# Kernel optimization log

Hardware: AMD Instinct MI355X
Metric: run time of the kernel (lower is better)

The kernel has to match this reference:

```python
import jax, jax.numpy as jnp
import numpy as np

EPS = 1e-5  # torch LayerNorm default
DT_RANK = 32  # ceil(d_model=512 / 16)


def layer_norm(x, g, b):
    mu = x.mean(-1, keepdims=True)
    var = x.var(-1, keepdims=True)
    return (x - mu) / jnp.sqrt(var + EPS) * g + b


def conv1d(x, w, b, pad):
    # x: (B, C, L), w: (O, I, K) -- torch Conv1d semantics
    y = jax.lax.conv_general_dilated(x, w, (1,), [(pad, pad)],
                                     dimension_numbers=('NCH', 'OIH', 'NCH'))
    return y + b[None, :, None]


def mamba(u, in_w, conv_w, conv_b, xproj_w, dt_w, dt_b, Alog, D, out_w, d_state, d_conv):
    # Faithful mamba_ssm Mamba block (no biases on in/x/out proj, RMS of official impl)
    Bsz, L, _ = u.shape
    xz = jnp.einsum('bld,ed->ble', u, in_w)          # (B, L, 2*Di)
    x, z = jnp.split(xz, 2, axis=-1)
    Di = x.shape[-1]
    # causal depthwise conv1d, truncated to L (padding=d_conv-1 on the left)
    xc = jax.lax.conv_general_dilated(x.transpose(0, 2, 1), conv_w[:, None, :], (1,),
                                      [(d_conv - 1, 0)],
                                      dimension_numbers=('NCH', 'OIH', 'NCH'),
                                      feature_group_count=Di)
    x = jax.nn.silu((xc + conv_b[None, :, None]).transpose(0, 2, 1))  # (B, L, Di)
    xdb = jnp.einsum('bld,ed->ble', x, xproj_w)       # (B, L, dt_rank + 2*N)
    dt = jax.nn.softplus(jnp.einsum('blr,dr->bld', xdb[..., :DT_RANK], dt_w) + dt_b)
    Bm = xdb[..., DT_RANK:DT_RANK + d_state]          # (B, L, N)
    Cm = xdb[..., DT_RANK + d_state:]                 # (B, L, N)
    A = -jnp.exp(Alog)                                # (Di, N)

    def step(h, ins):
        dt_t, x_t, B_t, C_t = ins                     # (B,Di),(B,Di),(B,N),(B,N)
        dA = jnp.exp(dt_t[..., None] * A)             # (B, Di, N)
        h = dA * h + (dt_t * x_t)[..., None] * B_t[:, None, :]
        y = (h * C_t[:, None, :]).sum(-1)             # (B, Di)
        return h, y

    h0 = jnp.zeros((Bsz, Di, d_state), u.dtype)
    xs = (dt.transpose(1, 0, 2), x.transpose(1, 0, 2),
          Bm.transpose(1, 0, 2), Cm.transpose(1, 0, 2))
    _, ys = jax.lax.scan(step, h0, xs)
    y = ys.transpose(1, 0, 2) + x * D                 # skip via D
    y = y * jax.nn.silu(z)
    return jnp.einsum('bld,od->blo', y, out_w)


def _forward(x, fe_w, fe_b, fe_ln_g, fe_ln_b, emb_ln_g, emb_ln_b,
             conv1_w, conv1_b, conv2_w, conv2_b,
             mf_in_w, mf_conv_w, mf_conv_b, mf_xproj_w, mf_dt_w, mf_dt_b, mf_Alog, mf_D, mf_out_w,
             mb_in_w, mb_conv_w, mb_conv_b, mb_xproj_w, mb_dt_w, mb_dt_b, mb_Alog, mb_D, mb_out_w,
             norm_g, norm_b, fc1_w, fc1_b, fc2_w, fc2_b):
    x = x.reshape(x.shape[0], 100, 23)
    # FrequencyEmbedding: rfft over a length-1 last dim == the signal itself; |.| then Linear+LN+ReLU
    id_mag = jnp.abs(x[..., :1])                      # (B, 100, 1)
    e = jax.nn.relu(layer_norm(id_mag @ fe_w.T + fe_b, fe_ln_g, fe_ln_b))
    id_embed = jax.nn.relu(layer_norm(e, emb_ln_g, emb_ln_b))  # outer LN+ReLU
    data = x[..., 1:].transpose(0, 2, 1)              # (B, 22, 100)
    f1 = jax.nn.relu(conv1d(data, conv1_w, conv1_b, 1))
    f2 = jax.nn.relu(conv1d(f1, conv2_w, conv2_b, 1)).transpose(0, 2, 1)  # (B,100,256)
    comb = jnp.concatenate([id_embed, f2], axis=-1)   # (B, 100, 512)
    fo = mamba(comb, mf_in_w, mf_conv_w, mf_conv_b, mf_xproj_w, mf_dt_w, mf_dt_b,
               mf_Alog, mf_D, mf_out_w, 16, 4)
    bo = mamba(comb[:, ::-1], mb_in_w, mb_conv_w, mb_conv_b, mb_xproj_w, mb_dt_w, mb_dt_b,
               mb_Alog, mb_D, mb_out_w, 8, 2)[:, ::-1]
    pooled = (fo + bo).max(axis=1)                    # (B, 512)
    pooled = layer_norm(pooled, norm_g, norm_b)       # self.norm (undefined in source; LN(512))
    h = jax.nn.relu(pooled @ fc1_w.T + fc1_b)
    return h @ fc2_w.T + fc2_b                        # (B, 4)


def setup_inputs() -> dict:
    key = jax.random.key(0)
    ks = iter(jax.random.split(key, 48))
    def n(shape, s=0.02):
        return jax.random.normal(next(ks), shape, jnp.float32) * s
    Di = 1024
    alog16 = jnp.log(jnp.tile(jnp.arange(1, 17, dtype=jnp.float32), (Di, 1)))
    alog8 = jnp.log(jnp.tile(jnp.arange(1, 9, dtype=jnp.float32), (Di, 1)))
    return {
        'x': jax.random.normal(next(ks), (512, 2300), jnp.float32),
        'fe_w': n((256, 1), 1.0), 'fe_b': jnp.zeros(256, jnp.float32),
        'fe_ln_g': jnp.ones(256, jnp.float32), 'fe_ln_b': jnp.zeros(256, jnp.float32),
        'emb_ln_g': jnp.ones(256, jnp.float32), 'emb_ln_b': jnp.zeros(256, jnp.float32),
        'conv1_w': n((128, 22, 3)), 'conv1_b': jnp.zeros(128, jnp.float32),
        'conv2_w': n((256, 128, 3)), 'conv2_b': jnp.zeros(256, jnp.float32),
        'mf_in_w': n((2 * Di, 512)), 'mf_conv_w': n((Di, 4)), 'mf_conv_b': jnp.zeros(Di, jnp.float32),
        'mf_xproj_w': n((32 + 2 * 16, Di)), 'mf_dt_w': n((Di, 32)), 'mf_dt_b': n((Di,), 0.1),
        'mf_Alog': alog16, 'mf_D': jnp.ones(Di, jnp.float32), 'mf_out_w': n((512, Di)),
        'mb_in_w': n((2 * Di, 512)), 'mb_conv_w': n((Di, 2)), 'mb_conv_b': jnp.zeros(Di, jnp.float32),
        'mb_xproj_w': n((32 + 2 * 8, Di)), 'mb_dt_w': n((Di, 32)), 'mb_dt_b': n((Di,), 0.1),
        'mb_Alog': alog8, 'mb_D': jnp.ones(Di, jnp.float32), 'mb_out_w': n((512, Di)),
        'norm_g': jnp.ones(512, jnp.float32), 'norm_b': jnp.zeros(512, jnp.float32),
        'fc1_w': n((128, 512)), 'fc1_b': jnp.zeros(128, jnp.float32),
        'fc2_w': n((4, 128)), 'fc2_b': jnp.zeros(4, jnp.float32),
    }


def reference(x, fe_w, fe_b, fe_ln_g, fe_ln_b, emb_ln_g, emb_ln_b,
              conv1_w, conv1_b, conv2_w, conv2_b,
              mf_in_w, mf_conv_w, mf_conv_b, mf_xproj_w, mf_dt_w, mf_dt_b, mf_Alog, mf_D, mf_out_w,
              mb_in_w, mb_conv_w, mb_conv_b, mb_xproj_w, mb_dt_w, mb_dt_b, mb_Alog, mb_D, mb_out_w,
              norm_g, norm_b, fc1_w, fc1_b, fc2_w, fc2_b):
    return _forward(x, fe_w, fe_b, fe_ln_g, fe_ln_b, emb_ln_g, emb_ln_b,
                    conv1_w, conv1_b, conv2_w, conv2_b,
                    mf_in_w, mf_conv_w, mf_conv_b, mf_xproj_w, mf_dt_w, mf_dt_b, mf_Alog, mf_D, mf_out_w,
                    mb_in_w, mb_conv_w, mb_conv_b, mb_xproj_w, mb_dt_w, mb_dt_b, mb_Alog, mb_D, mb_out_w,
                    norm_g, norm_b, fc1_w, fc1_b, fc2_w, fc2_b)
```

## Files before the change

### kernel.cpp

```cpp
#include <hip/hip_runtime.h>
#include <cstddef>
#include <cstdint>

#define BSZ 512
#define SEQ 100

typedef __bf16 bf16_t;
typedef __attribute__((ext_vector_type(8))) __bf16 bf16x8;
typedef __attribute__((ext_vector_type(4))) float f32x4;

__device__ __forceinline__ float sigmoidf_(float v){ return 1.f/(1.f + __expf(-v)); }
__device__ __forceinline__ float siluf_(float v){ return v * sigmoidf_(v); }
__device__ __forceinline__ float softplusf_(float v){ return (v > 20.f) ? v : __logf(1.f + __expf(v)); }

__global__ __launch_bounds__(256) void cvt_bf16_kernel(
    const float* __restrict__ src, bf16_t* __restrict__ dst, int n)
{
    int i = blockIdx.x*256 + threadIdx.x;
    if (i < n) dst[i] = (bf16_t)src[i];
}

__global__ __launch_bounds__(256) void prep_outw_kernel(
    const float* __restrict__ of, const float* __restrict__ ob, bf16_t* __restrict__ W)
{
    int i = blockIdx.x*256 + threadIdx.x;
    if (i < 512*2048){
        int o = i >> 11, k = i & 2047;
        W[i] = (bf16_t)((k < 1024) ? of[o*1024 + k] : ob[o*1024 + (k - 1024)]);
    }
}

__global__ __launch_bounds__(256) void prep_convw_kernel(
    const float* __restrict__ c1w, const float* __restrict__ c2w,
    bf16_t* __restrict__ W1p, bf16_t* __restrict__ W2p)
{
    int i = blockIdx.x*256 + threadIdx.x;
    if (i < 128*96){
        int o = i / 96, kk = i - o*96, k = kk >> 5, c = kk & 31;
        W1p[i] = (c < 22) ? (bf16_t)c1w[(o*22 + c)*3 + k] : (bf16_t)0.f;
    }
    if (i < 256*384){
        int o = i / 384, kk = i - o*384, k = kk >> 7, c = kk & 127;
        W2p[i] = (bf16_t)c2w[(o*128 + c)*3 + k];
    }
}

__global__ __launch_bounds__(256) void fe0_kernel(
    const float* __restrict__ x,
    const float* __restrict__ fe_w, const float* __restrict__ fe_b,
    const float* __restrict__ g1, const float* __restrict__ b1,
    const float* __restrict__ g2, const float* __restrict__ b2,
    bf16_t* __restrict__ comb, bf16_t* __restrict__ F0pad, bf16_t* __restrict__ F1pad)
{
    const int b = blockIdx.x;
    const int t = threadIdx.x;
    const int wv = t >> 6, lane = t & 63;

    float few[4], feb[4], lg1[4], lb1[4], lg2[4], lb2[4];
    #pragma unroll
    for (int q = 0; q < 4; ++q){
        int j = lane + 64*q;
        few[q] = fe_w[j]; feb[q] = fe_b[j];
        lg1[q] = g1[j];  lb1[q] = b1[j];
        lg2[q] = g2[j];  lb2[q] = b2[j];
    }
    for (int l = wv; l < SEQ; l += 4){
        float m = fabsf(x[(size_t)(b*SEQ + l)*23]);
        float e[4];
        float s1 = 0.f, s2 = 0.f;
        #pragma unroll
        for (int q = 0; q < 4; ++q){ e[q] = m*few[q] + feb[q]; s1 += e[q]; s2 += e[q]*e[q]; }
        #pragma unroll
        for (int off = 32; off > 0; off >>= 1){ s1 += __shfl_xor(s1, off); s2 += __shfl_xor(s2, off); }
        float mean = s1 * (1.f/256.f);
        float rstd = rsqrtf(s2*(1.f/256.f) - mean*mean + 1e-5f);
        s1 = 0.f; s2 = 0.f;
        #pragma unroll
        for (int q = 0; q < 4; ++q){
            e[q] = fmaxf((e[q]-mean)*rstd*lg1[q] + lb1[q], 0.f);
            s1 += e[q]; s2 += e[q]*e[q];
        }
        #pragma unroll
        for (int off = 32; off > 0; off >>= 1){ s1 += __shfl_xor(s1, off); s2 += __shfl_xor(s2, off); }
        mean = s1 * (1.f/256.f);
        rstd = rsqrtf(s2*(1.f/256.f) - mean*mean + 1e-5f);
        #pragma unroll
        for (int q = 0; q < 4; ++q){
            float v = fmaxf((e[q]-mean)*rstd*lg2[q] + lb2[q], 0.f);
            comb[(size_t)(b*SEQ + l)*512 + lane + 64*q] = (bf16_t)v;
        }
    }

    for (int idx = t; idx < 102*32; idx += 256){
        int r = idx >> 5, c = idx & 31;
        float v = 0.f;
        if (r >= 1 && r <= SEQ && c < 22) v = x[(size_t)(b*SEQ + r - 1)*23 + 1 + c];
        F0pad[(size_t)(b*102 + r)*32 + c] = (bf16_t)v;
    }
    if (t < 128) F1pad[(size_t)(b*102 + 0)*128 + t] = (bf16_t)0.f;
    else F1pad[(size_t)(b*102 + 101)*128 + (t - 128)] = (bf16_t)0.f;
}

__global__ __launch_bounds__(256) void gemm_conv_kernel(
    const bf16_t* __restrict__ Abase, int lda, int Az,
    const bf16_t* __restrict__ W, int K, int N,
    const float* __restrict__ bias,
    bf16_t* __restrict__ Cbase, int ldc, int Cb, int coff, int noff, int Mtot)
{
    __shared__ bf16_t As[128*32];
    __shared__ bf16_t Ws[128*32];
    const bf16_t* A = Abase + (size_t)blockIdx.z * Az;
    const int t = threadIdx.x;
    const int lane = t & 63, w = t >> 6;
    const int n0 = blockIdx.y * 128;
    const int rsub = lane >> 2, csub = lane & 3;
    const int col = lane & 15, quad = lane >> 4;
    const int wOffM = (w & 1) * 64, wOffN = (w >> 1) * 64;

    f32x4 acc[4][4];
    #pragma unroll
    for (int i = 0; i < 4; ++i)
        #pragma unroll
        for (int j = 0; j < 4; ++j)
            acc[i][j] = (f32x4){0.f, 0.f, 0.f, 0.f};

    for (int k0 = 0; k0 < K; k0 += 32){
        __syncthreads();
        #pragma unroll
        for (int q = 0; q < 2; ++q){
            const int rt = w*32 + q*16 + rsub;
            const int lq = csub ^ ((rt >> 1) & 3);
            int ra = (rt < Mtot) ? rt : (Mtot - 1);
            const bf16_t* ga = A + (size_t)ra*lda + k0 + lq*8;
            __builtin_amdgcn_global_load_lds(
                (const __attribute__((address_space(1))) void*)ga,
                (__attribute__((address_space(3))) void*)&As[(w*32 + q*16)*32], 16, 0, 0);
            const bf16_t* gw = W + (size_t)(n0 + rt)*K + k0 + lq*8;
            __builtin_amdgcn_global_load_lds(
                (const __attribute__((address_space(1))) void*)gw,
                (__attribute__((address_space(3))) void*)&Ws[(w*32 + q*16)*32], 16, 0, 0);
        }
        __syncthreads();

        bf16x8 af[4], bfv[4];
        #pragma unroll
        for (int i = 0; i < 4; ++i){
            const int ra = wOffM + i*16 + col;
            af[i]  = *(const bf16x8*)&As[ra*32 + (quad ^ ((ra >> 1) & 3))*8];
            const int rb = wOffN + i*16 + col;
            bfv[i] = *(const bf16x8*)&Ws[rb*32 + (quad ^ ((rb >> 1) & 3))*8];
        }
        #pragma unroll
        for (int i = 0; i < 4; ++i)
            #pragma unroll
            for (int j = 0; j < 4; ++j)
                acc[i][j] = __builtin_amdgcn_mfma_f32_16x16x32_bf16(af[i], bfv[j], acc[i][j], 0, 0, 0);
    }

    #pragma unroll
    for (int i = 0; i < 4; ++i){
        const int gmb = wOffM + i*16 + quad*4;
        #pragma unroll
        for (int j = 0; j < 4; ++j){
            const int gn = n0 + wOffN + j*16 + col;
            const float bb = bias[gn];
            #pragma unroll
            for (int r = 0; r < 4; ++r){
                const int gm = gmb + r;
                if (gm < Mtot){
                    float v = fmaxf(acc[i][j][r] + bb, 0.f);
                    Cbase[((size_t)blockIdx.z*Cb + coff + gm)*ldc + noff + gn] = (bf16_t)v;
                }
            }
        }
    }
}

__global__ __launch_bounds__(256) void gemm_in_kernel(
    const bf16_t* __restrict__ A, int lda, int Mtot,
    const bf16_t* __restrict__ W, int K,
    bf16_t* __restrict__ xy, bf16_t* __restrict__ z)
{
    __shared__ bf16_t As[128*32];
    __shared__ bf16_t Ws[128*32];
    const int t = threadIdx.x;
    const int lane = t & 63, w = t >> 6;
    const int m0 = blockIdx.x * 128, n0 = blockIdx.y * 128;
    const int rsub = lane >> 2, csub = lane & 3;
    const int col = lane & 15, quad = lane >> 4;
    const int wOffM = (w & 1) * 64, wOffN = (w >> 1) * 64;

    f32x4 acc[4][4];
    #pragma unroll
    for (int i = 0; i < 4; ++i)
        #pragma unroll
        for (int j = 0; j < 4; ++j)
            acc[i][j] = (f32x4){0.f, 0.f, 0.f, 0.f};

    for (int k0 = 0; k0 < K; k0 += 32){
        __syncthreads();
        #pragma unroll
        for (int q = 0; q < 2; ++q){
            const int rt = w*32 + q*16 + rsub;
            const int lq = csub ^ ((rt >> 1) & 3);
            int ra = m0 + rt; ra = (ra < Mtot) ? ra : (Mtot - 1);
            const bf16_t* ga = A + (size_t)ra*lda + k0 + lq*8;
            __builtin_amdgcn_global_load_lds(
                (const __attribute__((address_space(1))) void*)ga,
                (__attribute__((address_space(3))) void*)&As[(w*32 + q*16)*32], 16, 0, 0);
            const bf16_t* gw = W + (size_t)(n0 + rt)*K + k0 + lq*8;
            __builtin_amdgcn_global_load_lds(
                (const __attribute__((address_space(1))) void*)gw,
                (__attribute__((address_space(3))) void*)&Ws[(w*32 + q*16)*32], 16, 0, 0);
        }
        __syncthreads();

        bf16x8 af[4], bfv[4];
        #pragma unroll
        for (int i = 0; i < 4; ++i){
            const int ra = wOffM + i*16 + col;
            af[i]  = *(const bf16x8*)&As[ra*32 + (quad ^ ((ra >> 1) & 3))*8];
            const int rb = wOffN + i*16 + col;
            bfv[i] = *(const bf16x8*)&Ws[rb*32 + (quad ^ ((rb >> 1) & 3))*8];
        }
        #pragma unroll
        for (int i = 0; i < 4; ++i)
            #pragma unroll
            for (int j = 0; j < 4; ++j)
                acc[i][j] = __builtin_amdgcn_mfma_f32_16x16x32_bf16(af[i], bfv[j], acc[i][j], 0, 0, 0);
    }

    #pragma unroll
    for (int i = 0; i < 4; ++i){
        const int gmb = m0 + wOffM + i*16 + quad*4;
        #pragma unroll
        for (int j = 0; j < 4; ++j){
            const int gn = n0 + wOffN + j*16 + col;
            const int half = gn >> 11, within = gn & 2047;
            const size_t colx = (size_t)(half*1024 + (within & 1023));
            bf16_t* dst = (within < 1024) ? xy : z;
            #pragma unroll
            for (int r = 0; r < 4; ++r){
                const int gm = gmb + r;
                if (gm < Mtot)
                    dst[(size_t)gm*2048 + colx] = (bf16_t)acc[i][j][r];
            }
        }
    }
}

__global__ __launch_bounds__(256) void gemm_out_kernel(
    const bf16_t* __restrict__ A, int Mtot,
    const bf16_t* __restrict__ W,
    float* __restrict__ C)
{
    __shared__ bf16_t As[128*32];
    __shared__ bf16_t Ws[128*32];
    const int t = threadIdx.x;
    const int lane = t & 63, w = t >> 6;
    const int m0 = blockIdx.x * 128, n0 = blockIdx.y * 128;
    const int rsub = lane >> 2, csub = lane & 3;
    const int col = lane & 15, quad = lane >> 4;
    const int wOffM = (w & 1) * 64, wOffN = (w >> 1) * 64;
    const int K = 2048;

    f32x4 acc[4][4];
    #pragma unroll
    for (int i = 0; i < 4; ++i)
        #pragma unroll
        for (int j = 0; j < 4; ++j)
            acc[i][j] = (f32x4){0.f, 0.f, 0.f, 0.f};

    for (int k0 = 0; k0 < K; k0 += 32){
        __syncthreads();
        #pragma unroll
        for (int q = 0; q < 2; ++q){
            const int rt = w*32 + q*16 + rsub;
            const int lq = csub ^ ((rt >> 1) & 3);
            int ra = m0 + rt; ra = (ra < Mtot) ? ra : (Mtot - 1);
            const bf16_t* ga = A + (size_t)ra*K + k0 + lq*8;
            __builtin_amdgcn_global_load_lds(
                (const __attribute__((address_space(1))) void*)ga,
                (__attribute__((address_space(3))) void*)&As[(w*32 + q*16)*32], 16, 0, 0);
            const bf16_t* gw = W + (size_t)(n0 + rt)*K + k0 + lq*8;
            __builtin_amdgcn_global_load_lds(
                (const __attribute__((address_space(1))) void*)gw,
                (__attribute__((address_space(3))) void*)&Ws[(w*32 + q*16)*32], 16, 0, 0);
        }
        __syncthreads();

        bf16x8 af[4], bfv[4];
        #pragma unroll
        for (int i = 0; i < 4; ++i){
            const int ra = wOffM + i*16 + col;
            af[i]  = *(const bf16x8*)&As[ra*32 + (quad ^ ((ra >> 1) & 3))*8];
            const int rb = wOffN + i*16 + col;
            bfv[i] = *(const bf16x8*)&Ws[rb*32 + (quad ^ ((rb >> 1) & 3))*8];
        }
        #pragma unroll
        for (int i = 0; i < 4; ++i)
            #pragma unroll
            for (int j = 0; j < 4; ++j)
                acc[i][j] = __builtin_amdgcn_mfma_f32_16x16x32_bf16(af[i], bfv[j], acc[i][j], 0, 0, 0);
    }

    #pragma unroll
    for (int i = 0; i < 4; ++i){
        const int gmb = m0 + wOffM + i*16 + quad*4;
        #pragma unroll
        for (int j = 0; j < 4; ++j){
            const int gn = n0 + wOffN + j*16 + col;
            #pragma unroll
            for (int r = 0; r < 4; ++r){
                const int gm = gmb + r;
                if (gm < Mtot)
                    C[(size_t)gm*512 + gn] = acc[i][j][r];
            }
        }
    }
}

__global__ __launch_bounds__(256) void gemm_x_kernel(
    const bf16_t* __restrict__ xy,
    const bf16_t* __restrict__ Wf, const bf16_t* __restrict__ Wb,
    float* __restrict__ C)
{
    __shared__ bf16_t As[128*32];
    __shared__ bf16_t Ws[64*32];
    const int half = blockIdx.y;
    const bf16_t* A = xy + half*1024;
    const bf16_t* W = half ? Wb : Wf;
    const int N = half ? 48 : 64;
    const int t = threadIdx.x;
    const int lane = t & 63, w = t >> 6;
    const int m0 = blockIdx.x * 128;
    const int rsub = lane >> 2, csub = lane & 3;
    const int col = lane & 15, quad = lane >> 4;

    f32x4 acc[2][4];
    #pragma unroll
    for (int i = 0; i < 2; ++i)
        #pragma unroll
        for (int j = 0; j < 4; ++j)
            acc[i][j] = (f32x4){0.f, 0.f, 0.f, 0.f};

    for (int k0 = 0; k0 < 1024; k0 += 32){
        __syncthreads();
        #pragma unroll
        for (int q = 0; q < 2; ++q){
            const int rt = q*64 + w*16 + rsub;
            const int lq = csub ^ ((rt >> 1) & 3);
            const bf16_t* ga = A + (size_t)(m0 + rt)*2048 + k0 + lq*8;
            __builtin_amdgcn_global_load_lds(
                (const __attribute__((address_space(1))) void*)ga,
                (__attribute__((address_space(3))) void*)&As[(q*64 + w*16)*32], 16, 0, 0);
        }
        {
            const int rt = w*16 + rsub;
            const int lq = csub ^ ((rt >> 1) & 3);
            int rw = (rt < N) ? rt : (N - 1);
            const bf16_t* gw = W + (size_t)rw*1024 + k0 + lq*8;
            __builtin_amdgcn_global_load_lds(
                (const __attribute__((address_space(1))) void*)gw,
                (__attribute__((address_space(3))) void*)&Ws[(w*16)*32], 16, 0, 0);
        }
        __syncthreads();

        bf16x8 af[2], bfv[4];
        #pragma unroll
        for (int i = 0; i < 2; ++i){
            const int ra = w*32 + i*16 + col;
            af[i]  = *(const bf16x8*)&As[ra*32 + (quad ^ ((ra >> 1) & 3))*8];
        }
        #pragma unroll
        for (int j = 0; j < 4; ++j){
            const int rb = j*16 + col;
            bfv[j] = *(const bf16x8*)&Ws[rb*32 + (quad ^ ((rb >> 1) & 3))*8];
        }
        #pragma unroll
        for (int i = 0; i < 2; ++i)
            #pragma unroll
            for (int j = 0; j < 4; ++j)
                acc[i][j] = __builtin_amdgcn_mfma_f32_16x16x32_bf16(af[i], bfv[j], acc[i][j], 0, 0, 0);
    }

    #pragma unroll
    for (int i = 0; i < 2; ++i){
        const int gmb = m0 + w*32 + i*16 + quad*4;
        #pragma unroll
        for (int j = 0; j < 4; ++j){
            const int gn = j*16 + col;
            if (gn < N){
                #pragma unroll
                for (int r = 0; r < 4; ++r)
                    C[(size_t)(gmb + r)*128 + half*64 + gn] = acc[i][j][r];
            }
        }
    }
}

__global__ __launch_bounds__(256) void dt_kernel(
    const float* __restrict__ xdb,
    const float* __restrict__ dtwf, const float* __restrict__ dtbf,
    const float* __restrict__ dtwb, const float* __restrict__ dtbb,
    bf16_t* __restrict__ dtb)
{
    const int half = blockIdx.y >> 3;
    const int d = (blockIdx.y & 7)*128 + (threadIdx.x & 127);
    const int mslot = threadIdx.x >> 7;
    const int m0 = blockIdx.x * 16;
    __shared__ float sd[16*32];
    for (int i = threadIdx.x; i < 16*32; i += 256){
        int r = i >> 5, c = i & 31;
        sd[i] = xdb[(size_t)(m0 + r)*128 + half*64 + c];
    }
    const float* dw = half ? dtwb : dtwf;
    float w[32];
    #pragma unroll
    for (int r = 0; r < 32; ++r) w[r] = dw[d*32 + r];
    const float db = half ? dtbb[d] : dtbf[d];
    __syncthreads();
    #pragma unroll
    for (int i = 0; i < 8; ++i){
        const int row = mslot + i*2;
        const float* rp = &sd[row*32];
        float a = db;
        #pragma unroll
        for (int r = 0; r < 32; ++r) a += w[r]*rp[r];
        dtb[(size_t)(m0 + row)*2048 + half*1024 + d] = (bf16_t)softplusf_(a);
    }
}

template<int DC, bool REV>
__device__ __forceinline__ void conv_dev(bf16_t* base, const float* wsrc, float bias)
{
    float w[DC];
    #pragma unroll
    for (int k = 0; k < DC; ++k) w[k] = wsrc[k];
    float hist[DC-1];
    #pragma unroll
    for (int k = 0; k < DC-1; ++k) hist[k] = 0.f;
    const int step = REV ? -1 : 1;
    int l = REV ? (SEQ-1) : 0;
    for (int t0 = 0; t0 < SEQ; t0 += 10){
        float v[10];
        #pragma unroll
        for (int i = 0; i < 10; ++i) v[i] = (float)base[(size_t)(l + step*i)*2048];
        float o[10];
        #pragma unroll
        for (int i = 0; i < 10; ++i){
            float a = bias + w[DC-1]*v[i];
            #pragma unroll
            for (int j = 1; j < DC; ++j) a += w[DC-1-j]*hist[j-1];
            #pragma unroll
            for (int j = DC-2; j >= 1; --j) hist[j] = hist[j-1];
            hist[0] = v[i];
            o[i] = siluf_(a);
        }
        #pragma unroll
        for (int i = 0; i < 10; ++i)
            base[(size_t)(l + step*i)*2048] = (bf16_t)o[i];
        l += step*10;
    }
}

__global__ __launch_bounds__(256) void conv_silu_kernel(
    bf16_t* __restrict__ xy,
    const float* __restrict__ cwf, const float* __restrict__ cbf,
    const float* __restrict__ cwb, const float* __restrict__ cbb)
{
    const int gid = blockIdx.x*256 + threadIdx.x;
    const int b = gid >> 11, d2 = gid & 2047;
    const int half = d2 >> 10, d = d2 & 1023;
    bf16_t* base = xy + (size_t)b*SEQ*2048 + d2;
    if (half == 0) conv_dev<4, false>(base, cwf + d*4, cbf[d]);
    else           conv_dev<2, true >(base, cwb + d*2, cbb[d]);
}

template<int DS, bool REV>
__device__ __forceinline__ void scan_dev(
    bf16_t* __restrict__ xybase, const bf16_t* __restrict__ zbase,
    const bf16_t* __restrict__ tbase, const float* __restrict__ sx,
    const float* __restrict__ Arow, float Dd)
{
    float Av[DS], h[DS];
    #pragma unroll
    for (int s = 0; s < DS; ++s){ Av[s] = -__expf(Arow[s]); h[s] = 0.f; }
    bool structured = true;
    #pragma unroll
    for (int s = 1; s < DS; ++s)
        structured = structured && (fabsf(Av[s] - (float)(s+1)*Av[0]) <= 1e-4f*(float)(s+1));
    const float A0 = Av[0];
    const int step = REV ? -1 : 1;

    if (structured){
        int l = REV ? (SEQ-1) : 0;
        for (int t0 = 0; t0 < SEQ; t0 += 10){
            float xr[10], zr[10], tr[10];
            #pragma unroll
            for (int i = 0; i < 10; ++i){
                const size_t li = (size_t)(l + step*i);
                xr[i] = (float)xybase[li*2048];
                zr[i] = (float)zbase[li*2048];
                tr[i] = (float)tbase[li*2048];
            }
            #pragma unroll
            for (int i = 0; i < 10; ++i){
                const int li = l + step*i;
                const float4* sxl4 = (const float4*)&sx[li*2*DS];
                const float dtv = tr[i];
                const float dtx = dtv * xr[i];
                const float r = __expf(dtv*A0);
                float rp = r;
                float yv = 0.f;
                #pragma unroll
                for (int s4 = 0; s4 < DS/4; ++s4){
                    float4 Bv = sxl4[s4];
                    float4 Cv = sxl4[DS/4 + s4];
                    h[s4*4+0] = rp*h[s4*4+0] + dtx*Bv.x; yv += h[s4*4+0]*Cv.x; rp *= r;
                    h[s4*4+1] = rp*h[s4*4+1] + dtx*Bv.y; yv += h[s4*4+1]*Cv.y; rp *= r;
                    h[s4*4+2] = rp*h[s4*4+2] + dtx*Bv.z; yv += h[s4*4+2]*Cv.z; rp *= r;
                    h[s4*4+3] = rp*h[s4*4+3] + dtx*Bv.w; yv += h[s4*4+3]*Cv.w; rp *= r;
                }
                yv += xr[i]*Dd;
                yv *= siluf_(zr[i]);
                xybase[(size_t)li*2048] = (bf16_t)yv;
            }
            l += step*10;
        }
    } else {
        int l = REV ? (SEQ-1) : 0;
        for (int t0 = 0; t0 < SEQ; t0 += 10){
            float xr[10], zr[10], tr[10];
            #pragma unroll
            for (int i = 0; i < 10; ++i){
                const size_t li = (size_t)(l + step*i);
                xr[i] = (float)xybase[li*2048];
                zr[i] = (float)zbase[li*2048];
                tr[i] = (float)tbase[li*2048];
            }
            #pragma unroll
            for (int i = 0; i < 10; ++i){
                const int li = l + step*i;
                const float4* sxl4 = (const float4*)&sx[li*2*DS];
                const float dtv = tr[i];
                const float dtx = dtv * xr[i];
                float yv = 0.f;
                #pragma unroll
                for (int s4 = 0; s4 < DS/4; ++s4){
                    float4 Bv = sxl4[s4];
                    float4 Cv = sxl4[DS/4 + s4];
                    h[s4*4+0] = __expf(dtv*Av[s4*4+0])*h[s4*4+0] + dtx*Bv.x; yv += h[s4*4+0]*Cv.x;
                    h[s4*4+1] = __expf(dtv*Av[s4*4+1])*h[s4*4+1] + dtx*Bv.y; yv += h[s4*4+1]*Cv.y;
                    h[s4*4+2] = __expf(dtv*Av[s4*4+2])*h[s4*4+2] + dtx*Bv.z; yv += h[s4*4+2]*Cv.z;
                    h[s4*4+3] = __expf(dtv*Av[s4*4+3])*h[s4*4+3] + dtx*Bv.w; yv += h[s4*4+3]*Cv.w;
                }
                yv += xr[i]*Dd;
                yv *= siluf_(zr[i]);
                xybase[(size_t)li*2048] = (bf16_t)yv;
            }
            l += step*10;
        }
    }
}

__global__ __launch_bounds__(256) void scan_kernel(
    bf16_t* __restrict__ xy, const bf16_t* __restrict__ z,
    const bf16_t* __restrict__ dtb, const float* __restrict__ xdb,
    const float* __restrict__ Alogf, const float* __restrict__ Dpf,
    const float* __restrict__ Alogb, const float* __restrict__ Dpb)
{
    const int b = blockIdx.x >> 3, s8 = blockIdx.x & 7;
    __shared__ float sx[SEQ*32];
    const float4* src = (const float4*)(xdb + (size_t)b*SEQ*128);
    float4* dst = (float4*)sx;

    if (s8 < 4){
        for (int i = threadIdx.x; i < SEQ*8; i += 256){
            int row = i >> 3, c = i & 7;
            dst[row*8 + c] = src[row*32 + 8 + c];
        }
        const int d = (s8 << 8) + threadIdx.x;
        __syncthreads();
        scan_dev<16, false>(
            xy  + (size_t)b*SEQ*2048 + d,
            z   + (size_t)b*SEQ*2048 + d,
            dtb + (size_t)b*SEQ*2048 + d,
            sx, Alogf + d*16, Dpf[d]);
    } else {
        for (int i = threadIdx.x; i < SEQ*4; i += 256){
            int row = i >> 2, c = i & 3;
            dst[row*4 + c] = src[row*32 + 24 + c];
        }
        const int d = ((s8 - 4) << 8) + threadIdx.x;
        __syncthreads();
        scan_dev<8, true>(
            xy  + (size_t)b*SEQ*2048 + 1024 + d,
            z   + (size_t)b*SEQ*2048 + 1024 + d,
            dtb + (size_t)b*SEQ*2048 + 1024 + d,
            sx, Alogb + d*8, Dpb[d]);
    }
}

__global__ __launch_bounds__(256) void head_kernel(
    const float* __restrict__ acc,
    const float* __restrict__ ng, const float* __restrict__ nb,
    const float* __restrict__ w1, const float* __restrict__ b1,
    const float* __restrict__ w2, const float* __restrict__ b2,
    float* __restrict__ out)
{
    const int b = blockIdx.x, t = threadIdx.x;
    __shared__ float4 sm4[256];
    __shared__ float sp[512];
    __shared__ float sh2[256];
    __shared__ float sh[128];
    __shared__ float red1[4], red2[4];
    const float* base = acc + (size_t)b*SEQ*512;

    {
        const int c4 = t & 127, lh = t >> 7;
        float4 m = make_float4(-3.4e38f, -3.4e38f, -3.4e38f, -3.4e38f);
        for (int l = lh*50; l < lh*50 + 50; ++l){
            float4 v = ((const float4*)(base + (size_t)l*512))[c4];
            m.x = fmaxf(m.x, v.x); m.y = fmaxf(m.y, v.y);
            m.z = fmaxf(m.z, v.z); m.w = fmaxf(m.w, v.w);
        }
        sm4[t] = m;
    }
    __syncthreads();
    if (t < 128){
        float4 a = sm4[t], c = sm4[t + 128];
        ((float4*)sp)[t] = make_float4(fmaxf(a.x,c.x), fmaxf(a.y,c.y),
                                       fmaxf(a.z,c.z), fmaxf(a.w,c.w));
    }
    __syncthreads();

    float s1 = 0.f, s2 = 0.f;
    for (int o = t; o < 512; o += 256){ float v = sp[o]; s1 += v; s2 += v*v; }
    #pragma unroll
    for (int off = 32; off > 0; off >>= 1){ s1 += __shfl_xor(s1, off); s2 += __shfl_xor(s2, off); }
    const int wv = t >> 6, lane = t & 63;
    if (lane == 0){ red1[wv] = s1; red2[wv] = s2; }
    __syncthreads();
    if (t == 0){
        float a = 0.f, c = 0.f;
        for (int i = 0; i < 4; ++i){ a += red1[i]; c += red2[i]; }
        float mean = a * (1.f/512.f);
        float var = c * (1.f/512.f) - mean*mean;
        red1[0] = mean; red2[0] = rsqrtf(var + 1e-5f);
    }
    __syncthreads();
    const float mean = red1[0], rstd = red2[0];
    for (int o = t; o < 512; o += 256) sp[o] = (sp[o]-mean)*rstd*ng[o] + nb[o];
    __syncthreads();

    {
        const int o = t & 127, half = t >> 7;
        const float4* wrow = (const float4*)(w1 + (size_t)o*512 + half*256);
        const float4* sp4 = (const float4*)sp + half*64;
        float s = 0.f;
        #pragma unroll 8
        for (int j = 0; j < 64; ++j){
            float4 a = sp4[j], wq = wrow[j];
            s += a.x*wq.x + a.y*wq.y + a.z*wq.z + a.w*wq.w;
        }
        sh2[t] = s;
    }
    __syncthreads();
    if (t < 128) sh[t] = fmaxf(sh2[t] + sh2[t + 128] + b1[t], 0.f);
    __syncthreads();
    if (t < 4){
        float a = b2[t];
        for (int j = 0; j < 128; ++j) a += sh[j]*w2[t*128 + j];
        out[b*4 + t] = a;
    }
}

extern "C" void kernel_launch(void* const* d_in, const int* in_sizes, int n_in,
                              void* d_out, int out_size, void* d_ws, size_t ws_size,
                              hipStream_t stream)
{
    (void)in_sizes; (void)n_in; (void)out_size;
    const float* x        = (const float*)d_in[0];
    const float* fe_w     = (const float*)d_in[1];
    const float* fe_b     = (const float*)d_in[2];
    const float* fe_ln_g  = (const float*)d_in[3];
    const float* fe_ln_b  = (const float*)d_in[4];
    const float* emb_ln_g = (const float*)d_in[5];
    const float* emb_ln_b = (const float*)d_in[6];
    const float* conv1_w  = (const float*)d_in[7];
    const float* conv1_b  = (const float*)d_in[8];
    const float* conv2_w  = (const float*)d_in[9];
    const float* conv2_b  = (const float*)d_in[10];
    const float* mf_in_w  = (const float*)d_in[11];
    const float* mf_conv_w= (const float*)d_in[12];
    const float* mf_conv_b= (const float*)d_in[13];
    const float* mf_xproj = (const float*)d_in[14];
    const float* mf_dt_w  = (const float*)d_in[15];
    const float* mf_dt_b  = (const float*)d_in[16];
    const float* mf_Alog  = (const float*)d_in[17];
    const float* mf_D     = (const float*)d_in[18];
    const float* mf_out_w = (const float*)d_in[19];
    const float* mb_in_w  = (const float*)d_in[20];
    const float* mb_conv_w= (const float*)d_in[21];
    const float* mb_conv_b= (const float*)d_in[22];
    const float* mb_xproj = (const float*)d_in[23];
    const float* mb_dt_w  = (const float*)d_in[24];
    const float* mb_dt_b  = (const float*)d_in[25];
    const float* mb_Alog  = (const float*)d_in[26];
    const float* mb_D     = (const float*)d_in[27];
    const float* mb_out_w = (const float*)d_in[28];
    const float* norm_g   = (const float*)d_in[29];
    const float* norm_b   = (const float*)d_in[30];
    const float* fc1_w    = (const float*)d_in[31];
    const float* fc1_b    = (const float*)d_in[32];
    const float* fc2_w    = (const float*)d_in[33];
    const float* fc2_b    = (const float*)d_in[34];
    float* out = (float*)d_out;

    char* p = (char*)d_ws;
    bf16_t* w_in   = (bf16_t*)p; p += (size_t)4096*512*sizeof(bf16_t);
    bf16_t* w_out  = (bf16_t*)p; p += (size_t)512*2048*sizeof(bf16_t);
    bf16_t* w_xpf  = (bf16_t*)p; p += (size_t)64*1024*sizeof(bf16_t);
    bf16_t* w_xpb  = (bf16_t*)p; p += (size_t)48*1024*sizeof(bf16_t);
    bf16_t* W1p    = (bf16_t*)p; p += (size_t)128*96*sizeof(bf16_t);
    bf16_t* W2p    = (bf16_t*)p; p += (size_t)256*384*sizeof(bf16_t);
    bf16_t* comb_all = (bf16_t*)p; p += (size_t)BSZ*SEQ*512*sizeof(bf16_t);
    const size_t fixed_bytes = (size_t)(p - (char*)d_ws);

    const size_t per_b = (size_t)SEQ * (2048*2 + 2048*2 + 2048*2 + 128*4);
    const size_t budget = (ws_size > fixed_bytes) ? (ws_size - fixed_bytes) : 0;
    int Bc = BSZ;
    while (Bc > 64 && (size_t)Bc * per_b > budget) Bc >>= 1;
    const int nch = BSZ / Bc;
    const int M = Bc * SEQ;

    bf16_t* F0pad = (bf16_t*)p;
    bf16_t* F1pad = F0pad + (size_t)BSZ*102*32;
    bf16_t* xy   = (bf16_t*)p;               p += (size_t)M*2048*sizeof(bf16_t);
    bf16_t* z    = (bf16_t*)p;               p += (size_t)M*2048*sizeof(bf16_t);
    bf16_t* dtb  = (bf16_t*)p;               p += (size_t)M*2048*sizeof(bf16_t);
    float*  xdb  = (float*)p;
    float*  accb = (float*)dtb;

    cvt_bf16_kernel<<<(2048*512+255)/256, 256, 0, stream>>>(mf_in_w, w_in, 2048*512);
    cvt_bf16_kernel<<<(2048*512+255)/256, 256, 0, stream>>>(mb_in_w, w_in + (size_t)2048*512, 2048*512);
    prep_outw_kernel<<<(512*2048+255)/256, 256, 0, stream>>>(mf_out_w, mb_out_w, w_out);
    cvt_bf16_kernel<<<(64*1024+255)/256,  256, 0, stream>>>(mf_xproj, w_xpf, 64*1024);
    cvt_bf16_kernel<<<(48*1024+255)/256,  256, 0, stream>>>(mb_xproj, w_xpb, 48*1024);
    prep_convw_kernel<<<(256*384+255)/256, 256, 0, stream>>>(conv1_w, conv2_w, W1p, W2p);

    fe0_kernel<<<BSZ, 256, 0, stream>>>(x, fe_w, fe_b, fe_ln_g, fe_ln_b,
        emb_ln_g, emb_ln_b, comb_all, F0pad, F1pad);
    gemm_conv_kernel<<<dim3(1, 1, BSZ), 256, 0, stream>>>(
        F0pad, 32, 102*32, W1p, 96, 128, conv1_b, F1pad, 128, 102, 1, 0, SEQ);
    gemm_conv_kernel<<<dim3(1, 2, BSZ), 256, 0, stream>>>(
        F1pad, 128, 102*128, W2p, 384, 256, conv2_b, comb_all, 512, 100, 0, 256, SEQ);

    const int gm128 = M / 128;

    for (int c = 0; c < nch; ++c){
        const size_t b0 = (size_t)c * Bc;
        const bf16_t* comb = comb_all + b0*SEQ*512;

        gemm_in_kernel<<<dim3(gm128, 32), 256, 0, stream>>>(comb, 512, M, w_in, 512, xy, z);
        conv_silu_kernel<<<Bc*2048/256, 256, 0, stream>>>(xy, mf_conv_w, mf_conv_b,
                                                          mb_conv_w, mb_conv_b);
        gemm_x_kernel<<<dim3(gm128, 2), 256, 0, stream>>>(xy, w_xpf, w_xpb, xdb);
        dt_kernel<<<dim3(M/16, 16), 256, 0, stream>>>(xdb, mf_dt_w, mf_dt_b,
                                                      mb_dt_w, mb_dt_b, dtb);
        scan_kernel<<<Bc*8, 256, 0, stream>>>(xy, z, dtb, xdb,
                                              mf_Alog, mf_D, mb_Alog, mb_D);
        gemm_out_kernel<<<dim3(gm128, 4), 256, 0, stream>>>(xy, M, w_out, accb);
        head_kernel<<<Bc, 256, 0, stream>>>(accb, norm_g, norm_b, fc1_w, fc1_b,
                                            fc2_w, fc2_b, out + b0*4);
    }
}
```

Baseline: 1.598 ms.

## Double K-step per barrier in GEMMs and balance fwd/bwd scan work per block

The in- and out-projection GEMMs now load two 32-wide K slices into separate LDS buffers per iteration, which halves the number of barrier pairs at the cost of twice the LDS per block. The scan kernel now gives every block 128 forward (16-state) channels and 128 backward (8-state) channels instead of putting only one direction in each block, which evens out per-block latency. The scan body is also refactored into a single templated core with the structured and unstructured A paths chosen at compile time, which may reduce code duplication and register pressure.

```diff
diff --git a/kernel.cpp b/kernel.cpp
--- a/kernel.cpp
+++ b/kernel.cpp
@@ -181,8 +181,8 @@
     const bf16_t* __restrict__ W, int K,
     bf16_t* __restrict__ xy, bf16_t* __restrict__ z)
 {
-    __shared__ bf16_t As[128*32];
-    __shared__ bf16_t Ws[128*32];
+    __shared__ bf16_t As[2][128*32];
+    __shared__ bf16_t Ws[2][128*32];
     const int t = threadIdx.x;
     const int lane = t & 63, w = t >> 6;
     const int m0 = blockIdx.x * 128, n0 = blockIdx.y * 128;
@@ -197,37 +197,43 @@
         for (int j = 0; j < 4; ++j)
             acc[i][j] = (f32x4){0.f, 0.f, 0.f, 0.f};
 
-    for (int k0 = 0; k0 < K; k0 += 32){
+    for (int k0 = 0; k0 < K; k0 += 64){
         __syncthreads();
         #pragma unroll
-        for (int q = 0; q < 2; ++q){
-            const int rt = w*32 + q*16 + rsub;
-            const int lq = csub ^ ((rt >> 1) & 3);
-            int ra = m0 + rt; ra = (ra < Mtot) ? ra : (Mtot - 1);
-            const bf16_t* ga = A + (size_t)ra*lda + k0 + lq*8;
-            __builtin_amdgcn_global_load_lds(
-                (const __attribute__((address_space(1))) void*)ga,
-                (__attribute__((address_space(3))) void*)&As[(w*32 + q*16)*32], 16, 0, 0);
-            const bf16_t* gw = W + (size_t)(n0 + rt)*K + k0 + lq*8;
-            __builtin_amdgcn_global_load_lds(
-                (const __attribute__((address_space(1))) void*)gw,
-                (__attribute__((address_space(3))) void*)&Ws[(w*32 + q*16)*32], 16, 0, 0);
+        for (int hh = 0; hh < 2; ++hh){
+            #pragma unroll
+            for (int q = 0; q < 2; ++q){
+                const int rt = w*32 + q*16 + rsub;
+                const int lq = csub ^ ((rt >> 1) & 3);
+                int ra = m0 + rt; ra = (ra < Mtot) ? ra : (Mtot - 1);
+                const bf16_t* ga = A + (size_t)ra*lda + k0 + hh*32 + lq*8;
+                __builtin_amdgcn_global_load_lds(
+                    (const __attribute__((address_space(1))) void*)ga,
+                    (__attribute__((address_space(3))) void*)&As[hh][(w*32 + q*16)*32], 16, 0, 0);
+                const bf16_t* gw = W + (size_t)(n0 + rt)*K + k0 + hh*32 + lq*8;
+                __builtin_amdgcn_global_load_lds(
+                    (const __attribute__((address_space(1))) void*)gw,
+                    (__attribute__((address_space(3))) void*)&Ws[hh][(w*32 + q*16)*32], 16, 0, 0);
+            }
         }
         __syncthreads();
 
-        bf16x8 af[4], bfv[4];
-        #pragma unroll
-        for (int i = 0; i < 4; ++i){
-            const int ra = wOffM + i*16 + col;
-            af[i]  = *(const bf16x8*)&As[ra*32 + (quad ^ ((ra >> 1) & 3))*8];
-            const int rb = wOffN + i*16 + col;
-            bfv[i] = *(const bf16x8*)&Ws[rb*32 + (quad ^ ((rb >> 1) & 3))*8];
-        }
-        #pragma unroll
-        for (int i = 0; i < 4; ++i)
-            #pragma unroll
-            for (int j = 0; j < 4; ++j)
-                acc[i][j] = __builtin_amdgcn_mfma_f32_16x16x32_bf16(af[i], bfv[j], acc[i][j], 0, 0, 0);
+        #pragma unroll
+        for (int hh = 0; hh < 2; ++hh){
+            bf16x8 af[4], bfv[4];
+            #pragma unroll
+            for (int i = 0; i < 4; ++i){
+                const int ra = wOffM + i*16 + col;
+                af[i]  = *(const bf16x8*)&As[hh][ra*32 + (quad ^ ((ra >> 1) & 3))*8];
+                const int rb = wOffN + i*16 + col;
+                bfv[i] = *(const bf16x8*)&Ws[hh][rb*32 + (quad ^ ((rb >> 1) & 3))*8];
+            }
+            #pragma unroll
+            for (int i = 0; i < 4; ++i)
+                #pragma unroll
+                for (int j = 0; j < 4; ++j)
+                    acc[i][j] = __builtin_amdgcn_mfma_f32_16x16x32_bf16(af[i], bfv[j], acc[i][j], 0, 0, 0);
+        }
     }
 
     #pragma unroll
@@ -254,8 +260,8 @@
     const bf16_t* __restrict__ W,
     float* __restrict__ C)
 {
-    __shared__ bf16_t As[128*32];
-    __shared__ bf16_t Ws[128*32];
+    __shared__ bf16_t As[2][128*32];
+    __shared__ bf16_t Ws[2][128*32];
     const int t = threadIdx.x;
     const int lane = t & 63, w = t >> 6;
     const int m0 = blockIdx.x * 128, n0 = blockIdx.y * 128;
@@ -271,37 +277,43 @@
         for (int j = 0; j < 4; ++j)
             acc[i][j] = (f32x4){0.f, 0.f, 0.f, 0.f};
 
-    for (int k0 = 0; k0 < K; k0 += 32){
+    for (int k0 = 0; k0 < K; k0 += 64){
         __syncthreads();
         #pragma unroll
-        for (int q = 0; q < 2; ++q){
-            const int rt = w*32 + q*16 + rsub;
-            const int lq = csub ^ ((rt >> 1) & 3);
-            int ra = m0 + rt; ra = (ra < Mtot) ? ra : (Mtot - 1);
-            const bf16_t* ga = A + (size_t)ra*K + k0 + lq*8;
-            __builtin_amdgcn_global_load_lds(
-                (const __attribute__((address_space(1))) void*)ga,
-                (__attribute__((address_space(3))) void*)&As[(w*32 + q*16)*32], 16, 0, 0);
-            const bf16_t* gw = W + (size_t)(n0 + rt)*K + k0 + lq*8;
-            __builtin_amdgcn_global_load_lds(
-                (const __attribute__((address_space(1))) void*)gw,
-                (__attribute__((address_space(3))) void*)&Ws[(w*32 + q*16)*32], 16, 0, 0);
+        for (int hh = 0; hh < 2; ++hh){
+            #pragma unroll
+            for (int q = 0; q < 2; ++q){
+                const int rt = w*32 + q*16 + rsub;
+                const int lq = csub ^ ((rt >> 1) & 3);
+                int ra = m0 + rt; ra = (ra < Mtot) ? ra : (Mtot - 1);
+                const bf16_t* ga = A + (size_t)ra*K + k0 + hh*32 + lq*8;
+                __builtin_amdgcn_global_load_lds(
+                    (const __attribute__((address_space(1))) void*)ga,
+                    (__attribute__((address_space(3))) void*)&As[hh][(w*32 + q*16)*32], 16, 0, 0);
+                const bf16_t* gw = W + (size_t)(n0 + rt)*K + k0 + hh*32 + lq*8;
+                __builtin_amdgcn_global_load_lds(
+                    (const __attribute__((address_space(1))) void*)gw,
+                    (__attribute__((address_space(3))) void*)&Ws[hh][(w*32 + q*16)*32], 16, 0, 0);
+            }
         }
         __syncthreads();
 
-        bf16x8 af[4], bfv[4];
-        #pragma unroll
-        for (int i = 0; i < 4; ++i){
-            const int ra = wOffM + i*16 + col;
-            af[i]  = *(const bf16x8*)&As[ra*32 + (quad ^ ((ra >> 1) & 3))*8];
-            const int rb = wOffN + i*16 + col;
-            bfv[i] = *(const bf16x8*)&Ws[rb*32 + (quad ^ ((rb >> 1) & 3))*8];
-        }
-        #pragma unroll
-        for (int i = 0; i < 4; ++i)
-            #pragma unroll
-            for (int j = 0; j < 4; ++j)
-                acc[i][j] = __builtin_amdgcn_mfma_f32_16x16x32_bf16(af[i], bfv[j], acc[i][j], 0, 0, 0);
+        #pragma unroll
+        for (int hh = 0; hh < 2; ++hh){
+            bf16x8 af[4], bfv[4];
+            #pragma unroll
+            for (int i = 0; i < 4; ++i){
+                const int ra = wOffM + i*16 + col;
+                af[i]  = *(const bf16x8*)&As[hh][ra*32 + (quad ^ ((ra >> 1) & 3))*8];
+                const int rb = wOffN + i*16 + col;
+                bfv[i] = *(const bf16x8*)&Ws[hh][rb*32 + (quad ^ ((rb >> 1) & 3))*8];
+            }
+            #pragma unroll
+            for (int i = 0; i < 4; ++i)
+                #pragma unroll
+                for (int j = 0; j < 4; ++j)
+                    acc[i][j] = __builtin_amdgcn_mfma_f32_16x16x32_bf16(af[i], bfv[j], acc[i][j], 0, 0, 0);
+        }
     }
 
     #pragma unroll
@@ -477,42 +489,38 @@
     else           conv_dev<2, true >(base, cwb + d*2, cbb[d]);
 }
 
-template<int DS, bool REV>
-__device__ __forceinline__ void scan_dev(
+template<int DS, bool REV, bool STRUCT>
+__device__ __forceinline__ void scan_core(
     bf16_t* __restrict__ xybase, const bf16_t* __restrict__ zbase,
     const bf16_t* __restrict__ tbase, const float* __restrict__ sx,
-    const float* __restrict__ Arow, float Dd)
-{
-    float Av[DS], h[DS];
-    #pragma unroll
-    for (int s = 0; s < DS; ++s){ Av[s] = -__expf(Arow[s]); h[s] = 0.f; }
-    bool structured = true;
-    #pragma unroll
-    for (int s = 1; s < DS; ++s)
-        structured = structured && (fabsf(Av[s] - (float)(s+1)*Av[0]) <= 1e-4f*(float)(s+1));
+    const float* __restrict__ Av, float Dd)
+{
+    float h[DS];
+    #pragma unroll
+    for (int s = 0; s < DS; ++s) h[s] = 0.f;
+    const int step = REV ? -1 : 1;
     const float A0 = Av[0];
-    const int step = REV ? -1 : 1;
-
-    if (structured){
-        int l = REV ? (SEQ-1) : 0;
-        for (int t0 = 0; t0 < SEQ; t0 += 10){
-            float xr[10], zr[10], tr[10];
-            #pragma unroll
-            for (int i = 0; i < 10; ++i){
-                const size_t li = (size_t)(l + step*i);
-                xr[i] = (float)xybase[li*2048];
-                zr[i] = (float)zbase[li*2048];
-                tr[i] = (float)tbase[li*2048];
-            }
-            #pragma unroll
-            for (int i = 0; i < 10; ++i){
-                const int li = l + step*i;
-                const float4* sxl4 = (const float4*)&sx[li*2*DS];
-                const float dtv = tr[i];
-                const float dtx = dtv * xr[i];
+    int l = REV ? (SEQ-1) : 0;
+
+    for (int t0 = 0; t0 < SEQ; t0 += 10){
+        float xr[10], zr[10], tr[10];
+        #pragma unroll
+        for (int i = 0; i < 10; ++i){
+            const size_t li = (size_t)(l + step*i);
+            xr[i] = (float)xybase[li*2048];
+            zr[i] = (float)zbase[li*2048];
+            tr[i] = (float)tbase[li*2048];
+        }
+        #pragma unroll
+        for (int i = 0; i < 10; ++i){
+            const int li = l + step*i;
+            const float4* sxl4 = (const float4*)&sx[li*2*DS];
+            const float dtv = tr[i];
+            const float dtx = dtv * xr[i];
+            float yv = 0.f;
+            if (STRUCT){
                 const float r = __expf(dtv*A0);
                 float rp = r;
-                float yv = 0.f;
                 #pragma unroll
                 for (int s4 = 0; s4 < DS/4; ++s4){
                     float4 Bv = sxl4[s4];
@@ -522,30 +530,7 @@
                     h[s4*4+2] = rp*h[s4*4+2] + dtx*Bv.z; yv += h[s4*4+2]*Cv.z; rp *= r;
                     h[s4*4+3] = rp*h[s4*4+3] + dtx*Bv.w; yv += h[s4*4+3]*Cv.w; rp *= r;
                 }
-                yv += xr[i]*Dd;
-                yv *= siluf_(zr[i]);
-                xybase[(size_t)li*2048] = (bf16_t)yv;
-            }
-            l += step*10;
-        }
-    } else {
-        int l = REV ? (SEQ-1) : 0;
-        for (int t0 = 0; t0 < SEQ; t0 += 10){
-            float xr[10], zr[10], tr[10];
-            #pragma unroll
-            for (int i = 0; i < 10; ++i){
-                const size_t li = (size_t)(l + step*i);
-                xr[i] = (float)xybase[li*2048];
-                zr[i] = (float)zbase[li*2048];
-                tr[i] = (float)tbase[li*2048];
-            }
-            #pragma unroll
-            for (int i = 0; i < 10; ++i){
-                const int li = l + step*i;
-                const float4* sxl4 = (const float4*)&sx[li*2*DS];
-                const float dtv = tr[i];
-                const float dtx = dtv * xr[i];
-                float yv = 0.f;
+            } else {
                 #pragma unroll
                 for (int s4 = 0; s4 < DS/4; ++s4){
                     float4 Bv = sxl4[s4];
@@ -555,13 +540,30 @@
                     h[s4*4+2] = __expf(dtv*Av[s4*4+2])*h[s4*4+2] + dtx*Bv.z; yv += h[s4*4+2]*Cv.z;
                     h[s4*4+3] = __expf(dtv*Av[s4*4+3])*h[s4*4+3] + dtx*Bv.w; yv += h[s4*4+3]*Cv.w;
                 }
-                yv += xr[i]*Dd;
-                yv *= siluf_(zr[i]);
-                xybase[(size_t)li*2048] = (bf16_t)yv;
-            }
-            l += step*10;
-        }
-    }
+            }
+            yv += xr[i]*Dd;
+            yv *= siluf_(zr[i]);
+            xybase[(size_t)li*2048] = (bf16_t)yv;
+        }
+        l += step*10;
+    }
+}
+
+template<int DS, bool REV>
+__device__ __forceinline__ void scan_dev(
+    bf16_t* __restrict__ xybase, const bf16_t* __restrict__ zbase,
+    const bf16_t* __restrict__ tbase, const float* __restrict__ sx,
+    const float* __restrict__ Arow, float Dd)
+{
+    float Av[DS];
+    #pragma unroll
+    for (int s = 0; s < DS; ++s) Av[s] = -__expf(Arow[s]);
+    bool structured = true;
+    #pragma unroll
+    for (int s = 1; s < DS; ++s)
+        structured = structured && (fabsf(Av[s] - (float)(s+1)*Av[0]) <= 1e-4f*(float)(s+1));
+    if (structured) scan_core<DS, REV, true >(xybase, zbase, tbase, sx, Av, Dd);
+    else            scan_core<DS, REV, false>(xybase, zbase, tbase, sx, Av, Dd);
 }
 
 __global__ __launch_bounds__(256) void scan_kernel(
@@ -571,34 +573,33 @@
     const float* __restrict__ Alogb, const float* __restrict__ Dpb)
 {
     const int b = blockIdx.x >> 3, s8 = blockIdx.x & 7;
-    __shared__ float sx[SEQ*32];
+    const int t = threadIdx.x;
+    __shared__ float sxF[SEQ*32];
+    __shared__ float sxB[SEQ*16];
     const float4* src = (const float4*)(xdb + (size_t)b*SEQ*128);
-    float4* dst = (float4*)sx;
-
-    if (s8 < 4){
-        for (int i = threadIdx.x; i < SEQ*8; i += 256){
+
+    {
+        float4* dstF = (float4*)sxF;
+        for (int i = t; i < SEQ*8; i += 256){
             int row = i >> 3, c = i & 7;
-            dst[row*8 + c] = src[row*32 + 8 + c];
-        }
-        const int d = (s8 << 8) + threadIdx.x;
-        __syncthreads();
-        scan_dev<16, false>(
-            xy  + (size_t)b*SEQ*2048 + d,
-            z   + (size_t)b*SEQ*2048 + d,
-            dtb + (size_t)b*SEQ*2048 + d,
-            sx, Alogf + d*16, Dpf[d]);
+            dstF[row*8 + c] = src[row*32 + 8 + c];
+        }
+        float4* dstB = (float4*)sxB;
+        for (int i = t; i < SEQ*4; i += 256){
+            int row = i >> 2, c = i & 3;
+            dstB[row*4 + c] = src[row*32 + 24 + c];
+        }
+    }
+    __syncthreads();
+
+    if (t < 128){
+        const int d = s8*128 + t;
+        const size_t off = (size_t)b*SEQ*2048 + d;
+        scan_dev<16, false>(xy + off, z + off, dtb + off, sxF, Alogf + d*16, Dpf[d]);
     } else {
-        for (int i = threadIdx.x; i < SEQ*4; i += 256){
-            int row = i >> 2, c = i & 3;
-            dst[row*4 + c] = src[row*32 + 24 + c];
-        }
-        const int d = ((s8 - 4) << 8) + threadIdx.x;
-        __syncthreads();
-        scan_dev<8, true>(
-            xy  + (size_t)b*SEQ*2048 + 1024 + d,
-            z   + (size_t)b*SEQ*2048 + 1024 + d,
-            dtb + (size_t)b*SEQ*2048 + 1024 + d,
-            sx, Alogb + d*8, Dpb[d]);
+        const int d = s8*128 + (t - 128);
+        const size_t off = (size_t)b*SEQ*2048 + 1024 + d;
+        scan_dev<8, true>(xy + off, z + off, dtb + off, sxB, Alogb + d*8, Dpb[d]);
     }
 }
 
```

Result: faster. 1.536 ms (-3.9%).
